# Performance work log

Hardware: AMD Instinct MI355X
Metric: run time of the kernel (lower is better)

The kernel has to match this reference:

```python
import jax, jax.numpy as jnp
import numpy as np

# Dimensions
B, C, H, W = 4, 256, 64, 64
O = 256                      # out_channels
K = 3                        # kernel size
K2 = K * K
STRIDE = (1, 1)
PAD = 1
Ho = (H + 2 * PAD - K) // STRIDE[0] + 1   # 64
Wo = (W + 2 * PAD - K) // STRIDE[1] + 1   # 64


def setup_inputs() -> dict:
    key = jax.random.key(0)
    ks = jax.random.split(key, 5)
    x = jax.random.normal(ks[0], (B, C, H, W), jnp.float32)
    # NOTE: the torch module zero-inits offset/modulator convs; we use small
    # random weights so the deformable sampling path is actually exercised.
    offset_w = 0.02 * jax.random.normal(ks[1], (2 * K2, C, K, K), jnp.float32)
    offset_b = jnp.zeros((2 * K2,), jnp.float32)
    mod_w = 0.02 * jax.random.normal(ks[2], (K2, C, K, K), jnp.float32)
    mod_b = jnp.zeros((K2,), jnp.float32)
    weight = jax.random.normal(ks[3], (O, C, K, K), jnp.float32) / np.sqrt(C * K2)
    return {"x": x, "offset_w": offset_w, "offset_b": offset_b,
            "mod_w": mod_w, "mod_b": mod_b, "weight": weight}


def _conv(x, w, b):
    y = jax.lax.conv_general_dilated(
        x, w, window_strides=STRIDE, padding=[(PAD, PAD), (PAD, PAD)],
        dimension_numbers=("NCHW", "OIHW", "NCHW"))
    return y + b[None, :, None, None]


def _deform_conv2d(x, offset, mask, weight):
    """Modulated deformable conv v2 (torchvision semantics, zero padding)."""
    Bq, Cq, Hq, Wq = x.shape
    # offset channels are (dy, dx) pairs per kernel tap, row-major over kernel
    off = offset.reshape(Bq, K2, 2, Ho, Wo)
    ky, kx = jnp.meshgrid(jnp.arange(K), jnp.arange(K), indexing="ij")
    ky = ky.reshape(K2).astype(x.dtype)
    kx = kx.reshape(K2).astype(x.dtype)
    hy = (jnp.arange(Ho) * STRIDE[0] - PAD).astype(x.dtype)
    wx = (jnp.arange(Wo) * STRIDE[1] - PAD).astype(x.dtype)
    # sampling positions [B, K2, Ho, Wo]
    py = off[:, :, 0] + ky[None, :, None, None] + hy[None, None, :, None]
    px = off[:, :, 1] + kx[None, :, None, None] + wx[None, None, None, :]

    P = K2 * Ho * Wo
    xf = x.reshape(Bq, Cq, Hq * Wq)
    y0 = jnp.floor(py)
    x0 = jnp.floor(px)
    val = jnp.zeros((Bq, Cq, P), x.dtype)
    for dy in (0.0, 1.0):
        for dx in (0.0, 1.0):
            yc = y0 + dy
            xc = x0 + dx
            wgt = (1.0 - jnp.abs(py - yc)) * (1.0 - jnp.abs(px - xc))
            valid = (yc >= 0) & (yc < Hq) & (xc >= 0) & (xc < Wq)
            idx = (jnp.clip(yc, 0, Hq - 1) * Wq
                   + jnp.clip(xc, 0, Wq - 1)).astype(jnp.int32).reshape(Bq, P)
            g = jnp.take_along_axis(xf, idx[:, None, :], axis=2)  # [B,C,P]
            val = val + (wgt * valid.astype(x.dtype)).reshape(Bq, 1, P) * g
    # modulation mask is per kernel tap, shared across channels
    cols = (val * mask.reshape(Bq, 1, P)).reshape(Bq, Cq, K2, Ho * Wo)
    out = jnp.einsum("bckp,ock->bop", cols, weight.reshape(weight.shape[0], Cq, K2))
    return out.reshape(Bq, weight.shape[0], Ho, Wo)


def reference(x, offset_w, offset_b, mod_w, mod_b, weight):
    offset = _conv(x, offset_w, offset_b)
    mask = 2.0 * jax.nn.sigmoid(_conv(x, mod_w, mod_b))
    return _deform_conv2d(x, offset, mask, weight)
```

## Files before the change

kernel.cpp:

```cpp
#include <hip/hip_runtime.h>
#include <math.h>


constexpr int Bn = 4;
constexpr int Cn = 256;
constexpr int Hn = 64;
constexpr int Wn = 64;
constexpr int On = 256;
constexpr int PB = Hn * Wn;
constexpr int NCH = 27;

typedef __attribute__((ext_vector_type(8))) _Float16 f16x8;
typedef __attribute__((ext_vector_type(2))) _Float16 f16x2;
typedef __attribute__((ext_vector_type(4))) float f32x4;

union FragU { uint4 u; f16x8 h; };

__device__ inline ushort f2h(float f) {
    _Float16 h = (_Float16)f;
    return __builtin_bit_cast(ushort, h);
}
__device__ inline uint pkh(float a, float b) {
    return __builtin_bit_cast(uint, __builtin_amdgcn_cvt_pkrtz(a, b));
}
__device__ inline f16x2 u2h(uint u) { return __builtin_bit_cast(f16x2, u); }
__device__ inline uint h2u(f16x2 h) { return __builtin_bit_cast(uint, h); }

__global__ __launch_bounds__(256)
void nhwcpack_kernel(const float* __restrict__ x,
                     const float* __restrict__ w,
                     const float* __restrict__ offw,
                     const float* __restrict__ modw,
                     ushort* __restrict__ xhf,
                     ushort* __restrict__ wTb,
                     ushort* __restrict__ owf)
{
    const int bid = blockIdx.x;
    const int b = bid >> 7, seg = bid & 127;
    const int t = threadIdx.x;
    __shared__ float tile[32][257];

    const float* src = x + (size_t)b * Cn * PB + seg * 32;
    #pragma unroll 4
    for (int i = 0; i < 32; ++i) {
        const int idx = i * 256 + t;
        const int c = idx >> 5, p = idx & 31;
        tile[p][c] = src[(size_t)c * PB + p];
    }
    __syncthreads();

    const int pr = t & 127;
    const int r0 = (t >> 7) * 16;
    uint* dH = reinterpret_cast<uint*>(xhf + ((size_t)b * PB + seg * 32) * 256);
    #pragma unroll 4
    for (int i = 0; i < 16; ++i) {
        const int row = r0 + i;
        const float v0 = tile[row][2 * pr];
        const float v1 = tile[row][2 * pr + 1];
        dH[(size_t)row * 128 + pr] = pkh(v0, v1);
    }

    #pragma unroll 1
    for (int u = 0; u < 5; ++u) {
        int unit = (u < 4) ? bid * 4 + u : (bid < 256 ? 2048 + bid : -1);
        if (unit < 0) break;
        const int tap = unit >> 8, c = unit & 255;
        const int o = t;
        wTb[((size_t)(unit >> 3) * 256 + o) * 8 + (c & 7)] =
            f2h(w[((size_t)o * Cn + c) * 9 + tap]);
        if (o < 32) {
            float v = 0.f;
            if (o < 18)      v = offw[((size_t)o * Cn + c) * 9 + tap];
            else if (o < 27) v = modw[((size_t)(o - 18) * Cn + c) * 9 + tap];
            owf[((size_t)(unit >> 3) * 32 + o) * 8 + (c & 7)] = f2h(v);
        }
    }
}

__global__ __launch_bounds__(512, 1)
void offmask_tile_kernel(const ushort* __restrict__ xhf,
                         const float* __restrict__ offb,
                         const float* __restrict__ modb,
                         const ushort* __restrict__ owf,
                         float* __restrict__ offm)
{
    const int hw = blockIdx.x;
    const int blk = (hw & 7) * 32 + (hw >> 3);
    const int b = blk >> 6, row = blk & 63;
    const int t = threadIdx.x;
    const int lane = t & 63;
    const int wv  = t >> 6;
    const int l15 = lane & 15;
    const int g   = lane >> 4;
    const int mt  = wv >> 2;
    const int nt  = wv & 3;

    __shared__ ushort xt[3 * 66 * 256];
    uint4* lds4 = reinterpret_cast<uint4*>(xt);

    {
        const int c  = t >> 3;
        const int og = (t & 7) * 4;
        #pragma unroll 1
        for (int r = 0; r < 3; ++r) {
            const int ysrc = row - 1 + r;
            const int ci = c + 1;
            const int base = (r * 66 + ci) * 32;
            if (ysrc >= 0 && ysrc < Hn) {
                const uint4* src = reinterpret_cast<const uint4*>(
                    xhf + ((size_t)(b * PB + ysrc * 64 + c)) * 256);
                #pragma unroll
                for (int j = 0; j < 4; ++j) {
                    const int o = og + j;
                    lds4[base + (o ^ (ci & 7))] = src[o];
                }
            } else {
                const uint4 z = make_uint4(0u, 0u, 0u, 0u);
                #pragma unroll
                for (int j = 0; j < 4; ++j) {
                    const int o = og + j;
                    lds4[base + (o ^ (ci & 7))] = z;
                }
            }
        }
        if (t < 192) {
            const int r = t >> 6, idx = t & 63;
            const int ci = (idx >= 32) ? 65 : 0;
            const int o = idx & 31;
            lds4[(r * 66 + ci) * 32 + (o ^ (ci & 7))] =
                make_uint4(0u, 0u, 0u, 0u);
        }
    }
    __syncthreads();

    const uint4* owfV = reinterpret_cast<const uint4*>(owf);
    f32x4 acc = (f32x4){0.f, 0.f, 0.f, 0.f};
    const int pos = nt * 16 + l15;

    #pragma unroll 1
    for (int tap = 0; tap < 9; ++tap) {
        const int ty = tap / 3, tx = tap % 3;
        const int ci = pos + tx;
        const int cbase = (ty * 66 + ci) * 32;
        const int cx = ci & 7;

        uint4 aH[8];
        #pragma unroll
        for (int s = 0; s < 8; ++s) {
            const size_t kb = (size_t)((tap * 8 + s) * 4 + g) * 32 + mt * 16 + l15;
            aH[s] = owfV[kb];
        }

        #pragma unroll
        for (int s = 0; s < 8; ++s) {
            FragU aHH, bH;
            aHH.u = aH[s];
            bH.u = lds4[cbase + ((4 * s + g) ^ cx)];
            acc = __builtin_amdgcn_mfma_f32_16x16x32_f16(aHH.h, bH.h, acc, 0, 0, 0);
        }
    }

    #pragma unroll
    for (int j = 0; j < 4; ++j) {
        const int ch = mt * 16 + g * 4 + j;
        if (ch < NCH) {
            float v = acc[j];
            if (ch < 18) v += offb[ch];
            else         v = 2.f / (1.f + expf(-(v + modb[ch - 18])));
            offm[((size_t)(b * NCH + ch)) * PB + row * 64 + pos] = v;
        }
    }
}

__global__ __launch_bounds__(512, 2)
void deform_nhwc_kernel(const ushort* __restrict__ xhf,
                        const float* __restrict__ offm,
                        const ushort* __restrict__ wTb,
                        float* __restrict__ out)
{
    const int hw = blockIdx.x;
    const int blk = (hw & 7) * 32 + (hw >> 3);
    const int b = blk >> 6, row = blk & 63;
    const int p0 = row * 64;
    const int t = threadIdx.x;
    const int lane = t & 63;
    const int wv  = t >> 6;
    const int l15 = lane & 15;
    const int g   = lane >> 4;

    __shared__ int4  s_off[576];
    __shared__ uint4 s_wgt[576];
    __shared__ uint  cols[4][1024];

    for (int ti = t; ti < 576; ti += 512) {
        const int k = ti >> 6, pos = ti & 63;
        const int p = p0 + pos;
        const float dy = offm[((size_t)(b * NCH + 2 * k)) * PB + p];
        const float dx = offm[((size_t)(b * NCH + 2 * k + 1)) * PB + p];
        const float m  = offm[((size_t)(b * NCH + 18 + k)) * PB + p];
        const int ky = k / 3, kx = k % 3;
        const float py = dy + (float)(ky + row - 1);
        const float px = dx + (float)(kx + pos - 1);
        const float y0f = floorf(py), x0f = floorf(px);
        const float fy = py - y0f, fx = px - x0f;
        const int y0 = (int)y0f, x0i = (int)x0f;
        const int y1 = y0 + 1, x1 = x0i + 1;
        const bool vy0 = (y0 >= 0) && (y0 < Hn);
        const bool vy1 = (y1 >= 0) && (y1 < Hn);
        const bool vx0 = (x0i >= 0) && (x0i < Wn);
        const bool vx1 = (x1 >= 0) && (x1 < Wn);
        const int y0c = min(max(y0, 0), Hn - 1);
        const int y1c = min(max(y1, 0), Hn - 1);
        const int x0c = min(max(x0i, 0), Wn - 1);
        const int x1c = min(max(x1, 0), Wn - 1);
        s_off[ti] = make_int4(y0c * Wn + x0c, y0c * Wn + x1c,
                              y1c * Wn + x0c, y1c * Wn + x1c);
        const float w0 = (vy0 && vx0) ? (1.f - fy) * (1.f - fx) * m : 0.f;
        const float w1 = (vy0 && vx1) ? (1.f - fy) * fx * m : 0.f;
        const float w2 = (vy1 && vx0) ? fy * (1.f - fx) * m : 0.f;
        const float w3 = (vy1 && vx1) ? fy * fx * m : 0.f;
        s_wgt[ti] = make_uint4(pkh(w0, w0), pkh(w1, w1),
                               pkh(w2, w2), pkh(w3, w3));
    }
    __syncthreads();

    const ushort* xb = xhf + (size_t)b * PB * 256;
    const int posT = t >> 4;
    const int chq  = t & 15;
    const uint4* wvp = reinterpret_cast<const uint4*>(wTb);
    const int o0 = wv * 32;

    const int ws0 = posT * 16
        + 4 * ((chq >> 2) ^ (posT & 3) ^ ((posT >> 2) & 3)) + (chq & 3);

    int ri[4];
    #pragma unroll
    for (int nt = 0; nt < 4; ++nt) {
        const int p = nt * 16 + l15;
        ri[nt] = p * 4 + (g ^ (p & 3) ^ ((p >> 2) & 3));
    }

    f32x4 acc[2][4];
    #pragma unroll
    for (int ot = 0; ot < 2; ++ot)
        #pragma unroll
        for (int nt = 0; nt < 4; ++nt)
            acc[ot][nt] = (f32x4){0.f, 0.f, 0.f, 0.f};

    #pragma unroll 1
    for (int cch = 0; cch < 18; ++cch) {
        const int tap = cch >> 1, cc0 = (cch & 1) * 128;
        const int4  offA = s_off[tap * 64 + posT];
        const uint4 wgtA = s_wgt[tap * 64 + posT];
        const int4  offB = s_off[tap * 64 + posT + 32];
        const uint4 wgtB = s_wgt[tap * 64 + posT + 32];
        const ushort* xc = xb + cc0 + 2 * chq;

        uint qa[4], qb[4], qc[4], qd[4], ra[4], rb[4], rc[4], rd[4];
        #pragma unroll
        for (int s = 0; s < 4; ++s) {
            const int so = s * 32;
            qa[s] = *reinterpret_cast<const uint*>(xc + (size_t)offA.x * 256 + so);
            qb[s] = *reinterpret_cast<const uint*>(xc + (size_t)offA.y * 256 + so);
            qc[s] = *reinterpret_cast<const uint*>(xc + (size_t)offA.z * 256 + so);
            qd[s] = *reinterpret_cast<const uint*>(xc + (size_t)offA.w * 256 + so);
            ra[s] = *reinterpret_cast<const uint*>(xc + (size_t)offB.x * 256 + so);
            rb[s] = *reinterpret_cast<const uint*>(xc + (size_t)offB.y * 256 + so);
            rc[s] = *reinterpret_cast<const uint*>(xc + (size_t)offB.z * 256 + so);
            rd[s] = *reinterpret_cast<const uint*>(xc + (size_t)offB.w * 256 + so);
        }
        uint4 apre[4][2];
        #pragma unroll
        for (int s = 0; s < 4; ++s) {
            const int kb = (cch * 4 + s) * 4 + g;
            apre[s][0] = wvp[(size_t)kb * 256 + o0 + l15];
            apre[s][1] = wvp[(size_t)kb * 256 + o0 + 16 + l15];
        }

        __syncthreads();

        #pragma unroll
        for (int s = 0; s < 4; ++s) {
            f16x2 v = u2h(qa[s]) * u2h(wgtA.x);
            v += u2h(qb[s]) * u2h(wgtA.y);
            v += u2h(qc[s]) * u2h(wgtA.z);
            v += u2h(qd[s]) * u2h(wgtA.w);
            cols[s][ws0] = h2u(v);
            f16x2 u = u2h(ra[s]) * u2h(wgtB.x);
            u += u2h(rb[s]) * u2h(wgtB.y);
            u += u2h(rc[s]) * u2h(wgtB.z);
            u += u2h(rd[s]) * u2h(wgtB.w);
            cols[s][ws0 + 512] = h2u(u);
        }
        __syncthreads();

        #pragma unroll
        for (int s = 0; s < 4; ++s) {
            FragU a0, a1, bf[4];
            a0.u = apre[s][0]; a1.u = apre[s][1];
            #pragma unroll
            for (int nt = 0; nt < 4; ++nt)
                bf[nt].u = reinterpret_cast<const uint4*>(cols[s])[ri[nt]];
            #pragma unroll
            for (int nt = 0; nt < 4; ++nt) {
                acc[0][nt] = __builtin_amdgcn_mfma_f32_16x16x32_f16(
                    a0.h, bf[nt].h, acc[0][nt], 0, 0, 0);
                acc[1][nt] = __builtin_amdgcn_mfma_f32_16x16x32_f16(
                    a1.h, bf[nt].h, acc[1][nt], 0, 0, 0);
            }
        }
    }

    float* ob = out + (size_t)b * On * PB;
    #pragma unroll
    for (int ot = 0; ot < 2; ++ot)
        #pragma unroll
        for (int nt = 0; nt < 4; ++nt)
            #pragma unroll
            for (int j = 0; j < 4; ++j)
                ob[((size_t)(o0 + ot * 16 + g * 4 + j)) * PB
                   + p0 + nt * 16 + l15] = acc[ot][nt][j];
}

extern "C" void kernel_launch(void* const* d_in, const int* in_sizes, int n_in,
                              void* d_out, int out_size, void* d_ws, size_t ws_size,
                              hipStream_t stream)
{
    const float* x    = (const float*)d_in[0];
    const float* offw = (const float*)d_in[1];
    const float* offb = (const float*)d_in[2];
    const float* modw = (const float*)d_in[3];
    const float* modb = (const float*)d_in[4];
    const float* wgt  = (const float*)d_in[5];
    float* out = (float*)d_out;

    char* ws = (char*)d_ws;
    float*  offm = (float*)ws;
    ushort* wTb  = (ushort*)(ws + 1769472);
    ushort* owf  = (ushort*)(ws + 2949120);
    ushort* xhf  = (ushort*)(ws + 3244032);

    nhwcpack_kernel<<<dim3(512), dim3(256), 0, stream>>>(
        x, wgt, offw, modw, xhf, wTb, owf);
    offmask_tile_kernel<<<dim3(256), dim3(512), 0, stream>>>(
        xhf, offb, modb, owf, offm);
    deform_nhwc_kernel<<<dim3(256), dim3(512), 0, stream>>>(
        xhf, offm, wTb, out);
}
```

Before: 65.32 us.

## Software-pipeline deform gathers with double-buffered LDS columns and one barrier per chunk

New measurement: 61.98 us. -5.1%, faster.

```diff
diff --git a/kernel.cpp b/kernel.cpp
--- a/kernel.cpp
+++ b/kernel.cpp
@@ -172,7 +172,7 @@
     }
 }
 
-__global__ __launch_bounds__(512, 2)
+__global__ __launch_bounds__(512, 1)
 void deform_nhwc_kernel(const ushort* __restrict__ xhf,
                         const float* __restrict__ offm,
                         const ushort* __restrict__ wTb,
@@ -190,7 +190,7 @@
 
     __shared__ int4  s_off[576];
     __shared__ uint4 s_wgt[576];
-    __shared__ uint  cols[4][1024];
+    __shared__ uint  cols[2][4][1024];
 
     for (int ti = t; ti < 576; ti += 512) {
         const int k = ti >> 6, pos = ti & 63;
@@ -247,60 +247,61 @@
         for (int nt = 0; nt < 4; ++nt)
             acc[ot][nt] = (f32x4){0.f, 0.f, 0.f, 0.f};
 
-    #pragma unroll 1
-    for (int cch = 0; cch < 18; ++cch) {
+    auto LOADA = [&](int cch, uint4 (&ap)[4][2]) {
+        #pragma unroll
+        for (int s = 0; s < 4; ++s) {
+            const int kb = (cch * 4 + s) * 4 + g;
+            ap[s][0] = wvp[(size_t)kb * 256 + o0 + l15];
+            ap[s][1] = wvp[(size_t)kb * 256 + o0 + 16 + l15];
+        }
+    };
+
+    auto ISSUE = [&](int cch, uint (&gg)[32]) {
         const int tap = cch >> 1, cc0 = (cch & 1) * 128;
-        const int4  offA = s_off[tap * 64 + posT];
-        const uint4 wgtA = s_wgt[tap * 64 + posT];
-        const int4  offB = s_off[tap * 64 + posT + 32];
-        const uint4 wgtB = s_wgt[tap * 64 + posT + 32];
+        const int4 oA = s_off[tap * 64 + posT];
+        const int4 oB = s_off[tap * 64 + posT + 32];
         const ushort* xc = xb + cc0 + 2 * chq;
-
-        uint qa[4], qb[4], qc[4], qd[4], ra[4], rb[4], rc[4], rd[4];
         #pragma unroll
         for (int s = 0; s < 4; ++s) {
             const int so = s * 32;
-            qa[s] = *reinterpret_cast<const uint*>(xc + (size_t)offA.x * 256 + so);
-            qb[s] = *reinterpret_cast<const uint*>(xc + (size_t)offA.y * 256 + so);
-            qc[s] = *reinterpret_cast<const uint*>(xc + (size_t)offA.z * 256 + so);
-            qd[s] = *reinterpret_cast<const uint*>(xc + (size_t)offA.w * 256 + so);
-            ra[s] = *reinterpret_cast<const uint*>(xc + (size_t)offB.x * 256 + so);
-            rb[s] = *reinterpret_cast<const uint*>(xc + (size_t)offB.y * 256 + so);
-            rc[s] = *reinterpret_cast<const uint*>(xc + (size_t)offB.z * 256 + so);
-            rd[s] = *reinterpret_cast<const uint*>(xc + (size_t)offB.w * 256 + so);
-        }
-        uint4 apre[4][2];
+            gg[s * 8 + 0] = *reinterpret_cast<const uint*>(xc + (size_t)oA.x * 256 + so);
+            gg[s * 8 + 1] = *reinterpret_cast<const uint*>(xc + (size_t)oA.y * 256 + so);
+            gg[s * 8 + 2] = *reinterpret_cast<const uint*>(xc + (size_t)oA.z * 256 + so);
+            gg[s * 8 + 3] = *reinterpret_cast<const uint*>(xc + (size_t)oA.w * 256 + so);
+            gg[s * 8 + 4] = *reinterpret_cast<const uint*>(xc + (size_t)oB.x * 256 + so);
+            gg[s * 8 + 5] = *reinterpret_cast<const uint*>(xc + (size_t)oB.y * 256 + so);
+            gg[s * 8 + 6] = *reinterpret_cast<const uint*>(xc + (size_t)oB.z * 256 + so);
+            gg[s * 8 + 7] = *reinterpret_cast<const uint*>(xc + (size_t)oB.w * 256 + so);
+        }
+    };
+
+    auto COMBINE = [&](int cch, const uint (&gg)[32], uint* cbuf) {
+        const int tap = cch >> 1;
+        const uint4 wgtA = s_wgt[tap * 64 + posT];
+        const uint4 wgtB = s_wgt[tap * 64 + posT + 32];
         #pragma unroll
         for (int s = 0; s < 4; ++s) {
-            const int kb = (cch * 4 + s) * 4 + g;
-            apre[s][0] = wvp[(size_t)kb * 256 + o0 + l15];
-            apre[s][1] = wvp[(size_t)kb * 256 + o0 + 16 + l15];
-        }
-
-        __syncthreads();
-
-        #pragma unroll
-        for (int s = 0; s < 4; ++s) {
-            f16x2 v = u2h(qa[s]) * u2h(wgtA.x);
-            v += u2h(qb[s]) * u2h(wgtA.y);
-            v += u2h(qc[s]) * u2h(wgtA.z);
-            v += u2h(qd[s]) * u2h(wgtA.w);
-            cols[s][ws0] = h2u(v);
-            f16x2 u = u2h(ra[s]) * u2h(wgtB.x);
-            u += u2h(rb[s]) * u2h(wgtB.y);
-            u += u2h(rc[s]) * u2h(wgtB.z);
-            u += u2h(rd[s]) * u2h(wgtB.w);
-            cols[s][ws0 + 512] = h2u(u);
-        }
-        __syncthreads();
-
+            f16x2 v = u2h(gg[s * 8 + 0]) * u2h(wgtA.x);
+            v += u2h(gg[s * 8 + 1]) * u2h(wgtA.y);
+            v += u2h(gg[s * 8 + 2]) * u2h(wgtA.z);
+            v += u2h(gg[s * 8 + 3]) * u2h(wgtA.w);
+            cbuf[s * 1024 + ws0] = h2u(v);
+            f16x2 u = u2h(gg[s * 8 + 4]) * u2h(wgtB.x);
+            u += u2h(gg[s * 8 + 5]) * u2h(wgtB.y);
+            u += u2h(gg[s * 8 + 6]) * u2h(wgtB.z);
+            u += u2h(gg[s * 8 + 7]) * u2h(wgtB.w);
+            cbuf[s * 1024 + ws0 + 512] = h2u(u);
+        }
+    };
+
+    auto MFMAS = [&](const uint* cbuf, const uint4 (&ap)[4][2]) {
         #pragma unroll
         for (int s = 0; s < 4; ++s) {
             FragU a0, a1, bf[4];
-            a0.u = apre[s][0]; a1.u = apre[s][1];
+            a0.u = ap[s][0]; a1.u = ap[s][1];
             #pragma unroll
             for (int nt = 0; nt < 4; ++nt)
-                bf[nt].u = reinterpret_cast<const uint4*>(cols[s])[ri[nt]];
+                bf[nt].u = reinterpret_cast<const uint4*>(cbuf + s * 1024)[ri[nt]];
             #pragma unroll
             for (int nt = 0; nt < 4; ++nt) {
                 acc[0][nt] = __builtin_amdgcn_mfma_f32_16x16x32_f16(
@@ -309,6 +310,32 @@
                     a1.h, bf[nt].h, acc[1][nt], 0, 0, 0);
             }
         }
+    };
+
+    uint  gA[32], gB[32];
+    uint4 aA[4][2], aB[4][2];
+
+    LOADA(0, aA);
+    ISSUE(0, gA);
+    #pragma unroll 1
+    for (int jj = 0; jj < 9; ++jj) {
+        LOADA(2 * jj + 1, aB);
+        ISSUE(2 * jj + 1, gB);
+        COMBINE(2 * jj, gA, &cols[0][0][0]);
+        asm volatile("s_waitcnt lgkmcnt(0)" ::: "memory");
+        __builtin_amdgcn_s_barrier();
+        asm volatile("" ::: "memory");
+        MFMAS(&cols[0][0][0], aA);
+
+        if (jj < 8) {
+            LOADA(2 * jj + 2, aA);
+            ISSUE(2 * jj + 2, gA);
+        }
+        COMBINE(2 * jj + 1, gB, &cols[1][0][0]);
+        asm volatile("s_waitcnt lgkmcnt(0)" ::: "memory");
+        __builtin_amdgcn_s_barrier();
+        asm volatile("" ::: "memory");
+        MFMAS(&cols[1][0][0], aB);
     }
 
     float* ob = out + (size_t)b * On * PB;
```
